# Performance work log

Hardware: AMD Instinct MI355X
Metric: run time of the kernel (lower is better)

The kernel has to match this reference:

```python
import jax, jax.numpy as jnp
import numpy as np

EPS = 1e-20
TEMP = 0.07
PATCH = 64
STEP = 32  # patch_size * overlap(0.5)


def zero_softmax(x, eps=1e-5):
    # ZeroSoftmax: ((exp(x)-1)^2) / (sum + eps), maps x==0 -> exactly 0 weight
    e = jnp.square(jnp.exp(x) - 1.0)
    return e / (jnp.sum(e, axis=-1, keepdims=True) + eps)


def _scaling_mask(H, W, p, step):
    # constant overlap-count mask from CRW.compute_scaling_mask (static shapes)
    sm = np.zeros((H, W), np.float32)
    for i in range(0, H - step, step):
        for j in range(0, W - step, step):
            sm[i:i + p, j:j + p] += 1.0
    return jnp.asarray(sm)


def _window_sums(m, p, step):
    # m: (B,T,SP,H,W) -> sliding-window sums (B,T,SP,nH,nW) via integral image
    ii = jnp.cumsum(jnp.cumsum(m, axis=-2), axis=-1)
    ii = jnp.pad(ii, ((0, 0), (0, 0), (0, 0), (1, 0), (1, 0)))
    H = m.shape[-2]
    nH = (H - p) // step + 1
    lo = jnp.arange(nH) * step
    hi = lo + p
    r_hi = ii[..., hi, :]   # (B,T,SP,nH,W+1)
    r_lo = ii[..., lo, :]
    return r_hi[..., hi] - r_hi[..., lo] - r_lo[..., hi] + r_lo[..., lo]


def setup_inputs() -> dict:
    key = jax.random.key(0)
    k1, k2, k3 = jax.random.split(key, 3)
    B, T, H, W = 2, 4, 256, 256
    nH = (H - PATCH) // STEP + 1  # 7
    N = nH * nH                   # 49 patches
    Cenc, D, SP = 512, 128, 64
    feats = jax.random.normal(k1, (B, N, Cenc, T), jnp.float32)
    W_head = jax.random.normal(k2, (Cenc, D), jnp.float32) / np.sqrt(Cenc)
    sp_mask = jax.random.randint(k3, (B, T, H, W), 0, SP, jnp.int32)
    return {"feats": feats, "W_head": W_head, "sp_mask": sp_mask, "max_sp_num": SP}


def reference(feats, W_head, sp_mask, max_sp_num):
    B, N, Cenc, T = feats.shape
    H, W = sp_mask.shape[-2:]
    SP = max_sp_num

    # --- pixels_to_nodes tail: projection head + L2 normalize over channel dim ---
    q = jnp.einsum('bnct,cd->bndt', feats, W_head)            # (B,N,128,T)
    nrm = jnp.maximum(jnp.linalg.norm(q, axis=2, keepdims=True), 1e-12)
    q = q / nrm
    q = jnp.transpose(q, (0, 2, 3, 1))                        # (B,128,T,N)

    # --- patches_to_sp_embeddings: windowed superpixel pooling ---
    oh = (sp_mask[:, :, None, :, :] ==
          jnp.arange(SP, dtype=sp_mask.dtype)[None, None, :, None, None]
          ).astype(jnp.float32)                               # (B,T,SP,H,W)
    sm = _scaling_mask(H, W, PATCH, STEP)                     # (H,W)
    ws = _window_sums(oh / sm, PATCH, STEP)                   # (B,T,SP,nH,nW)
    denom = jnp.sum(oh, axis=(-1, -2)) + EPS                  # (B,T,SP)
    wts = jnp.transpose(ws, (0, 1, 3, 4, 2)) / denom[:, :, None, None, :]
    wts = wts.reshape(B, T, N, SP)                            # (B,T,N,SP)
    q_sp = jnp.einsum('bdtn,btns->bdts', q, wts)              # (B,128,T,SP)

    # --- affinity + zero_softmax stochastic matrices ---
    As = jnp.einsum('bdtn,bdtm->btnm', q_sp[:, :, :-1], q_sp[:, :, 1:])  # (B,T-1,SP,SP)
    A12 = zero_softmax(As / TEMP)
    A21 = zero_softmax(jnp.swapaxes(As, -1, -2) / TEMP)

    # --- palindrome random walks + cross-entropy to cycle-consistency targets ---
    tgt = jnp.tile(jnp.arange(SP), B)
    loss = jnp.float32(0.0)
    AAs = []
    for i in range(1, T - 1):
        mats = [A12[:, k] for k in range(i + 1)] + [A21[:, k] for k in range(i, -1, -1)]
        aa = mats[0]
        for m in mats[1:]:
            aa = aa @ m
        AAs.append(aa)
        logits = jnp.log(aa + EPS).reshape(B * SP, SP)
        logp = jax.nn.log_softmax(logits, axis=-1)
        loss = loss + jnp.mean(-logp[jnp.arange(B * SP), tgt])
    return loss, jnp.stack(AAs)
```

## Files before the change

### kernel.cpp

```cpp
#include <hip/hip_runtime.h>
#include <hip/hip_bf16.h>

constexpr int NWIN = 49;
constexpr int QLD  = 52;

constexpr int OFF_Q    = 26624;
constexpr int OFF_QSP  = 79872;
constexpr int OFF_A12T = 169984;
constexpr int OFF_A21  = 194560;
constexpr int OFF_A21T = 219136;
constexpr int OFF_R1T  = 251904;
constexpr int OFF_L    = 260096;
constexpr int OFF_BAR  = 276480;
constexpr int OFF_H    = 276608;

__global__ void __launch_bounds__(256, 1)
k_front(const int* __restrict__ mask, const float* __restrict__ feats,
        const float* __restrict__ Wh, float* __restrict__ h, float* __restrict__ q) {
    if (blockIdx.x < 98) {
        int bid = blockIdx.x;
        int n = bid % NWIN, b = bid / NWIN;
        __shared__ float4 f4[512];
        __shared__ float4 psum4[8 * 129];
        __shared__ float4 red4[2];
        const float4* fp4 = (const float4*)(feats + (size_t)(b * NWIN + n) * 2048);
        for (int i = threadIdx.x; i < 512; i += 256) f4[i] = fp4[i];
        __syncthreads();

        int dl = threadIdx.x & 31, ch = threadIdx.x >> 5;
        const float4* wh4 = (const float4*)Wh;
        float a0x=0.f,a0y=0.f,a0z=0.f,a0w=0.f;
        float a1x=0.f,a1y=0.f,a1z=0.f,a1w=0.f;
        float a2x=0.f,a2y=0.f,a2z=0.f,a2w=0.f;
        float a3x=0.f,a3y=0.f,a3z=0.f,a3w=0.f;
        int c0 = ch * 64;
        #pragma unroll 8
        for (int cc = 0; cc < 64; ++cc) {
            int c = c0 + cc;
            float4 w4 = wh4[c * 32 + dl];
            float4 fv = f4[c];
            a0x += fv.x * w4.x; a0y += fv.y * w4.x; a0z += fv.z * w4.x; a0w += fv.w * w4.x;
            a1x += fv.x * w4.y; a1y += fv.y * w4.y; a1z += fv.z * w4.y; a1w += fv.w * w4.y;
            a2x += fv.x * w4.z; a2y += fv.y * w4.z; a2z += fv.z * w4.z; a2w += fv.w * w4.z;
            a3x += fv.x * w4.w; a3y += fv.y * w4.w; a3z += fv.z * w4.w; a3w += fv.w * w4.w;
        }
        psum4[ch * 129 + dl * 4 + 0] = make_float4(a0x, a0y, a0z, a0w);
        psum4[ch * 129 + dl * 4 + 1] = make_float4(a1x, a1y, a1z, a1w);
        psum4[ch * 129 + dl * 4 + 2] = make_float4(a2x, a2y, a2z, a2w);
        psum4[ch * 129 + dl * 4 + 3] = make_float4(a3x, a3y, a3z, a3w);
        __syncthreads();

        float4 A;
        if (threadIdx.x < 128) {
            int d = threadIdx.x;
            A = psum4[d];
            #pragma unroll
            for (int c = 1; c < 8; ++c) {
                float4 p = psum4[c * 129 + d];
                A.x += p.x; A.y += p.y; A.z += p.z; A.w += p.w;
            }
            float sx = A.x * A.x, sy = A.y * A.y, sz = A.z * A.z, sw = A.w * A.w;
            for (int off = 32; off; off >>= 1) {
                sx += __shfl_down(sx, off); sy += __shfl_down(sy, off);
                sz += __shfl_down(sz, off); sw += __shfl_down(sw, off);
            }
            if ((threadIdx.x & 63) == 0) red4[threadIdx.x >> 6] = make_float4(sx, sy, sz, sw);
        }
        __syncthreads();
        if (threadIdx.x < 128) {
            float4 r0 = red4[0], r1 = red4[1];
            float ix = 1.f / fmaxf(sqrtf(r0.x + r1.x), 1e-12f);
            float iy = 1.f / fmaxf(sqrtf(r0.y + r1.y), 1e-12f);
            float iz = 1.f / fmaxf(sqrtf(r0.z + r1.z), 1e-12f);
            float iw = 1.f / fmaxf(sqrtf(r0.w + r1.w), 1e-12f);
            float* qb = q + (size_t)(b * 128 + (int)threadIdx.x) * 4 * QLD + n;
            qb[0 * QLD] = A.x * ix;
            qb[1 * QLD] = A.y * iy;
            qb[2 * QLD] = A.z * iz;
            qb[3 * QLD] = A.w * iw;
        }
    } else {
        int blkc = blockIdx.x - 98;
        int bt = blkc >> 6, cell = blkc & 63;
        int cy = cell >> 3, cx = cell & 7;
        __shared__ float loc[64];
        if (threadIdx.x < 64) loc[threadIdx.x] = 0.f;
        __syncthreads();
        const int* base = mask + bt * 65536 + (cy * 32) * 256 + cx * 32;
        #pragma unroll
        for (int it = 0; it < 4; ++it) {
            int idx = it * 256 + (int)threadIdx.x;
            int r = idx >> 5, c = idx & 31;
            int s = base[r * 256 + c];
            atomicAdd(&loc[s], 1.f);
        }
        __syncthreads();
        if (threadIdx.x < 64)
            h[(size_t)(bt * 64 + cell) * 64 + threadIdx.x] = loc[threadIdx.x];
    }
}

__global__ void k_qsp(const float* __restrict__ q, const float* __restrict__ hg,
                      float* __restrict__ qsp, float* __restrict__ out,
                      int* __restrict__ bar) {
    if (blockIdx.x == 0 && threadIdx.x < 4) {
        bar[threadIdx.x] = 0;
        if (threadIdx.x == 0) out[0] = 0.f;
    }
    int gid0 = blockIdx.x * 256;
    int t = (gid0 >> 13) & 3;
    int b = gid0 >> 15;
    int bt = b * 4 + t;
    int sbase = (gid0 >> 7) & 63;

    __shared__ float wrow[2][52];
    {
        int grp = threadIdx.x >> 7;
        int w = threadIdx.x & 127;
        if (w < 52) {
            float v = 0.f;
            if (w < 49) {
                int wy = w / 7, wx = w % 7;
                int s = sbase + grp;
                const float* hb = hg + (size_t)bt * 4096 + s;
                float wr0 = (wy >= 1 && wy <= 6) ? 0.5f : 1.f;
                float wr1 = (wy <= 5) ? 0.5f : 1.f;
                float wc0 = (wx >= 1 && wx <= 6) ? 0.5f : 1.f;
                float wc1 = (wx <= 5) ? 0.5f : 1.f;
                v = wr0 * wc0 * hb[(wy * 8 + wx) * 64]
                  + wr0 * wc1 * hb[(wy * 8 + wx + 1) * 64]
                  + wr1 * wc0 * hb[((wy + 1) * 8 + wx) * 64]
                  + wr1 * wc1 * hb[((wy + 1) * 8 + wx + 1) * 64];
            }
            wrow[grp][w] = v;
        }
    }
    __syncthreads();

    int tid = gid0 + threadIdx.x;
    int d = tid & 127;
    int s = (tid >> 7) & 63;
    const float4* qrow = (const float4*)(q + (size_t)((b * 128 + d) * 4 + t) * QLD);
    const float4* wr4 = (const float4*)wrow[threadIdx.x >> 7];
    float acc = 0.f, den = 0.f;
    #pragma unroll
    for (int i = 0; i < 13; ++i) {
        float4 w = wr4[i];
        float4 qv = qrow[i];
        den += w.x + w.y + w.z + w.w;
        acc += qv.x * w.x + qv.y * w.y + qv.z * w.z + qv.w * w.w;
    }
    int w = (s * 32 + ((d >> 2) ^ (s & 31))) * 4 + (d & 3);
    qsp[(size_t)bt * 8192 + w] = acc / (den + 1e-20f);
}


__device__ __forceinline__ void dump_mat(float* M, const float4* v) {
    #pragma unroll
    for (int it = 0; it < 4; ++it) {
        int idx = it * 256 + (int)threadIdx.x;
        int r = idx >> 4, c4 = (idx & 15) << 2;
        *(float4*)&M[r * 64 + (c4 ^ ((r & 15) << 2))] = v[it];
    }
}

__device__ __forceinline__ void stage1(float* M, const float* __restrict__ G) {
    const float4* g = (const float4*)G;
    float4 v[4];
    #pragma unroll
    for (int it = 0; it < 4; ++it) v[it] = g[it * 256 + (int)threadIdx.x];
    dump_mat(M, v);
}

__device__ __forceinline__ void mm256_sw(float* acc, const float* Ra, const float* Rb) {
    int tid = threadIdx.x;
    int nl = tid >> 4, ml = tid & 15;
    int sxa = nl << 2, sxb = ml << 2;
    #pragma unroll
    for (int i = 0; i < 16; ++i) acc[i] = 0.f;
    #pragma unroll 4
    for (int k0 = 0; k0 < 64; k0 += 4) {
        float4 av[4], bv[4];
        #pragma unroll
        for (int i = 0; i < 4; ++i)
            av[i] = *(const float4*)&Ra[(nl + 16 * i) * 64 + (k0 ^ sxa)];
        #pragma unroll
        for (int j = 0; j < 4; ++j)
            bv[j] = *(const float4*)&Rb[(ml + 16 * j) * 64 + (k0 ^ sxb)];
        #pragma unroll
        for (int i = 0; i < 4; ++i)
            #pragma unroll
            for (int j = 0; j < 4; ++j)
                acc[i * 4 + j] += av[i].x * bv[j].x + av[i].y * bv[j].y
                                + av[i].z * bv[j].z + av[i].w * bv[j].w;
    }
}

__device__ __forceinline__ void wr256_sw(float* M, const float* acc) {
    int nl = threadIdx.x >> 4, ml = threadIdx.x & 15;
    #pragma unroll
    for (int i = 0; i < 4; ++i)
        #pragma unroll
        for (int j = 0; j < 4; ++j) {
            int r = nl + 16 * i, k = ml + 16 * j;
            M[r * 64 + (((k & ~3) ^ ((r & 15) << 2)) | (k & 3))] = acc[i * 4 + j];
        }
}

__device__ __forceinline__ void store_mat(float* __restrict__ G, const float* acc) {
    int nl = threadIdx.x >> 4, ml = threadIdx.x & 15;
    #pragma unroll
    for (int i = 0; i < 4; ++i)
        #pragma unroll
        for (int j = 0; j < 4; ++j)
            G[(nl + 16 * i) * 64 + ml + 16 * j] = acc[i * 4 + j];
}

__device__ __forceinline__ void store_loss(const float* acc, float* __restrict__ aa,
                                           float* __restrict__ out, float* red) {
    int tid = threadIdx.x;
    int nl = tid >> 4, ml = tid & 15;
    #pragma unroll
    for (int i = 0; i < 4; ++i)
        #pragma unroll
        for (int j = 0; j < 4; ++j)
            aa[(nl + 16 * i) * 64 + (ml + 16 * j)] = acc[i * 4 + j];
    int l = tid & 63;
    float part = 0.f;
    #pragma unroll
    for (int i = 0; i < 4; ++i) {
        float rsum = acc[i * 4 + 0] + acc[i * 4 + 1] + acc[i * 4 + 2] + acc[i * 4 + 3];
        rsum += __shfl_down(rsum, 8, 16);
        rsum += __shfl_down(rsum, 4, 16);
        rsum += __shfl_down(rsum, 2, 16);
        rsum += __shfl_down(rsum, 1, 16);
        float dv = __shfl(acc[5 * i], (l & 48) | nl, 64);
        if ((l & 15) == 0) part += logf(rsum + 6.4e-19f) - logf(dv + 1e-20f);
    }
    for (int off = 32; off; off >>= 1) part += __shfl_down(part, off);
    if (l == 0) red[tid >> 6] = part;
    __syncthreads();
    if (tid == 0) atomicAdd(out, (red[0] + red[1] + red[2] + red[3]) * (1.f / 128.f));
}

__device__ __forceinline__ void gbar(int* cnt, int target) {
    __syncthreads();
    if (threadIdx.x == 0) {
        __threadfence();
        __hip_atomic_fetch_add(cnt, 1, __ATOMIC_ACQ_REL, __HIP_MEMORY_SCOPE_AGENT);
        while (__hip_atomic_load(cnt, __ATOMIC_ACQUIRE, __HIP_MEMORY_SCOPE_AGENT) < target)
            __builtin_amdgcn_s_sleep(2);
        __threadfence();
    }
    __syncthreads();
}

__global__ void __launch_bounds__(256, 1)
k_tail(const float* __restrict__ qsp,
       float* __restrict__ a12T, float* __restrict__ a21, float* __restrict__ a21T,
       float* __restrict__ wsR1T, float* __restrict__ wsL,
       float* __restrict__ out, int* __restrict__ bar) {
    __shared__ float SM[16384];
    float* M0 = SM;
    float* M1 = SM + 4096;
    float* M2 = SM + 8192;
    float* M3 = SM + 12288;
    const int tid = threadIdx.x;
    const int blk = blockIdx.x;
    const int t = blk % 3, b = blk / 3;

    {
        float4* qaT4 = (float4*)SM;
        float4* qbT4 = (float4*)SM + 2048;
        {
            const float4* gA = (const float4*)(qsp + (size_t)(b * 4 + t) * 8192);
            const float4* gB = (const float4*)(qsp + (size_t)(b * 4 + t + 1) * 8192);
            #pragma unroll
            for (int it = 0; it < 8; ++it) {
                int idx = it * 256 + tid;
                qaT4[idx] = gA[idx];
                qbT4[idx] = gB[idx];
            }
        }
        __syncthreads();

        const int nl = tid >> 4, ml = tid & 15;
        float acc[16];
        #pragma unroll
        for (int i = 0; i < 16; ++i) acc[i] = 0.f;
        #pragma unroll 8
        for (int k4 = 0; k4 < 32; ++k4) {
            float4 av[4], bv[4];
            #pragma unroll
            for (int i = 0; i < 4; ++i) { int n = nl + 16 * i; av[i] = qaT4[n * 32 + (k4 ^ (n & 31))]; }
            #pragma unroll
            for (int j = 0; j < 4; ++j) { int m = ml + 16 * j; bv[j] = qbT4[m * 32 + (k4 ^ (m & 31))]; }
            #pragma unroll
            for (int i = 0; i < 4; ++i)
                #pragma unroll
                for (int j = 0; j < 4; ++j)
                    acc[i * 4 + j] += av[i].x * bv[j].x + av[i].y * bv[j].y
                                    + av[i].z * bv[j].z + av[i].w * bv[j].w;
        }
        __syncthreads();

        float* eb = (float*)qaT4;
        float* rs = (float*)qbT4;
        float* cs = rs + 64;
        #pragma unroll
        for (int i = 0; i < 4; ++i)
            #pragma unroll
            for (int j = 0; j < 4; ++j) {
                int n = nl + 16 * i, m = ml + 16 * j;
                float x = acc[i * 4 + j] * (1.f / 0.07f);
                float e = expf(x) - 1.f;
                eb[n * 65 + m] = e * e;
            }
        __syncthreads();
        if (tid < 128) {
            int r = tid & 63; bool isrow = tid < 64;
            float a = 0.f;
            #pragma unroll
            for (int k = 0; k < 64; ++k) a += isrow ? eb[r * 65 + k] : eb[k * 65 + r];
            (isrow ? rs : cs)[r] = a + 1e-5f;
        }
        __syncthreads();
        float* p12T = a12T + (b * 3 + t) * 4096;
        float* p21  = a21  + (b * 3 + t) * 4096;
        float* p21T = a21T + (b * 3 + t) * 4096;
        #pragma unroll
        for (int i = 0; i < 4; ++i)
            #pragma unroll
            for (int j = 0; j < 4; ++j) {
                int n = nl + 16 * i, m = ml + 16 * j;
                float v   = eb[n * 65 + m];
                float v12 = v / rs[n];
                float v21 = v / cs[m];
                if (t == 0) {
                    M3[n * 64 + (((m & ~3) ^ ((n & 15) << 2)) | (m & 3))] = v12;
                    p21T[n * 64 + m] = v21;
                } else if (t == 1) {
                    p12T[m * 64 + n] = v12;
                    M3[m * 64 + (((n & ~3) ^ ((m & 15) << 2)) | (n & 3))] = v21;
                } else {
                    p12T[m * 64 + n] = v12;
                    p21 [m * 64 + n] = v21;
                }
            }
    }
    gbar(bar + 0, 6);
    if (t == 2) return;
    const bool odd = (t == 1);

    if (!odd) {
        stage1(M0, a12T + (b * 3 + 1) * 4096);
        __syncthreads();
        float accP[16];
        mm256_sw(accP, M3, M0);
        wr256_sw(M1, accP);
        stage1(M2, a12T + (b * 3 + 2) * 4096);
        __syncthreads();
        float accL[16];
        mm256_sw(accL, M1, M2);
        store_mat(wsL + b * 4096, accL);
    } else {
        stage1(M0, a21T + (b * 3 + 0) * 4096);
        __syncthreads();
        float accR[16];
        mm256_sw(accR, M0, M3);
        store_mat(wsR1T + b * 4096, accR);
        wr256_sw(M1, accR);
        stage1(M2, a21 + (b * 3 + 2) * 4096);
        __syncthreads();
        float accRT[16];
        mm256_sw(accRT, M1, M2);
        wr256_sw(M0, accRT);
    }
    gbar(bar + 1, 4);

    if (!odd) {
        stage1(M2, wsR1T + b * 4096);
        __syncthreads();
        float acc[16];
        mm256_sw(acc, M1, M2);
        store_loss(acc, out + 1 + b * 4096, out, M0);
    } else {
        stage1(M2, wsL + b * 4096);
        __syncthreads();
        float acc[16];
        mm256_sw(acc, M2, M0);
        store_loss(acc, out + 1 + (2 + b) * 4096, out, M1);
    }
}

extern "C" void kernel_launch(void* const* d_in, const int* in_sizes, int n_in,
                              void* d_out, int out_size, void* d_ws, size_t ws_size,
                              hipStream_t stream) {
    const float* feats = (const float*)d_in[0];
    const float* Wh    = (const float*)d_in[1];
    const int*   mask  = (const int*)d_in[2];
    float* out = (float*)d_out;
    float* ws  = (float*)d_ws;

    float* q       = ws + OFF_Q;
    float* qsp     = ws + OFF_QSP;
    float* a12T    = ws + OFF_A12T;
    float* a21     = ws + OFF_A21;
    float* a21T    = ws + OFF_A21T;
    float* wsR1T   = ws + OFF_R1T;
    float* wsL     = ws + OFF_L;
    float* h       = ws + OFF_H;
    int*   bar     = (int*)(ws + OFF_BAR);

    k_front<<<98 + 512, 256, 0, stream>>>(mask, feats, Wh, h, q);
    k_qsp<<<256, 256, 0, stream>>>(q, h, qsp, out, bar);
    k_tail<<<6, 256, 0, stream>>>(qsp, a12T, a21, a21T,
                                  wsR1T, wsL, out, bar);
}
```

Baseline: 100.1 us.

## Use half-block 64x64 matmuls and overlap next-operand staging with compute in tail kernel

The 64x64 matrix products in the tail kernel now run on only the first 128 threads, each computing a 8x4 register tile. The other 128 threads load the next operand matrix from global memory into shared memory at the same time, which removes one __syncthreads and hides load latency. The affinity GEMM is also moved to 128 threads. The risk is that half the threads sit idle during compute and per-thread register pressure doubles, so throughput per matmul may fall.

```diff
diff --git a/kernel.cpp b/kernel.cpp
--- a/kernel.cpp
+++ b/kernel.cpp
@@ -155,7 +155,11 @@
 }
 
 
-__device__ __forceinline__ void dump_mat(float* M, const float4* v) {
+__device__ __forceinline__ void stage1(float* M, const float* __restrict__ G) {
+    const float4* g = (const float4*)G;
+    float4 v[4];
+    #pragma unroll
+    for (int it = 0; it < 4; ++it) v[it] = g[it * 256 + (int)threadIdx.x];
     #pragma unroll
     for (int it = 0; it < 4; ++it) {
         int idx = it * 256 + (int)threadIdx.x;
@@ -164,31 +168,34 @@
     }
 }
 
-__device__ __forceinline__ void stage1(float* M, const float* __restrict__ G) {
+__device__ __forceinline__ void stage1_h(float* M, const float* __restrict__ G) {
+    int lt = (int)threadIdx.x - 128;
     const float4* g = (const float4*)G;
-    float4 v[4];
-    #pragma unroll
-    for (int it = 0; it < 4; ++it) v[it] = g[it * 256 + (int)threadIdx.x];
-    dump_mat(M, v);
-}
-
-__device__ __forceinline__ void mm256_sw(float* acc, const float* Ra, const float* Rb) {
-    int tid = threadIdx.x;
-    int nl = tid >> 4, ml = tid & 15;
-    int sxa = nl << 2, sxb = ml << 2;
-    #pragma unroll
-    for (int i = 0; i < 16; ++i) acc[i] = 0.f;
-    #pragma unroll 4
+    #pragma unroll
+    for (int it = 0; it < 8; ++it) {
+        int idx = it * 128 + lt;
+        int r = idx >> 4, c4 = (idx & 15) << 2;
+        *(float4*)&M[r * 64 + (c4 ^ ((r & 15) << 2))] = g[idx];
+    }
+}
+
+__device__ __forceinline__ void mm128_sw(float* acc, const float* Ra, const float* Rb) {
+    int lt = threadIdx.x;
+    int nl = lt >> 4, ml = lt & 15;
+    int sxa0 = nl << 2, sxa1 = (nl + 8) << 2, sxb = ml << 2;
+    #pragma unroll
+    for (int i = 0; i < 32; ++i) acc[i] = 0.f;
+    #pragma unroll 2
     for (int k0 = 0; k0 < 64; k0 += 4) {
-        float4 av[4], bv[4];
-        #pragma unroll
-        for (int i = 0; i < 4; ++i)
-            av[i] = *(const float4*)&Ra[(nl + 16 * i) * 64 + (k0 ^ sxa)];
+        float4 av[8], bv[4];
+        #pragma unroll
+        for (int i = 0; i < 8; ++i)
+            av[i] = *(const float4*)&Ra[(nl + 8 * i) * 64 + (k0 ^ ((i & 1) ? sxa1 : sxa0))];
         #pragma unroll
         for (int j = 0; j < 4; ++j)
             bv[j] = *(const float4*)&Rb[(ml + 16 * j) * 64 + (k0 ^ sxb)];
         #pragma unroll
-        for (int i = 0; i < 4; ++i)
+        for (int i = 0; i < 8; ++i)
             #pragma unroll
             for (int j = 0; j < 4; ++j)
                 acc[i * 4 + j] += av[i].x * bv[j].x + av[i].y * bv[j].y
@@ -196,51 +203,53 @@
     }
 }
 
-__device__ __forceinline__ void wr256_sw(float* M, const float* acc) {
+__device__ __forceinline__ void wr128_sw(float* M, const float* acc) {
     int nl = threadIdx.x >> 4, ml = threadIdx.x & 15;
     #pragma unroll
-    for (int i = 0; i < 4; ++i)
+    for (int i = 0; i < 8; ++i)
         #pragma unroll
         for (int j = 0; j < 4; ++j) {
-            int r = nl + 16 * i, k = ml + 16 * j;
+            int r = nl + 8 * i, k = ml + 16 * j;
             M[r * 64 + (((k & ~3) ^ ((r & 15) << 2)) | (k & 3))] = acc[i * 4 + j];
         }
 }
 
-__device__ __forceinline__ void store_mat(float* __restrict__ G, const float* acc) {
+__device__ __forceinline__ void store_mat128(float* __restrict__ G, const float* acc) {
     int nl = threadIdx.x >> 4, ml = threadIdx.x & 15;
     #pragma unroll
-    for (int i = 0; i < 4; ++i)
+    for (int i = 0; i < 8; ++i)
         #pragma unroll
         for (int j = 0; j < 4; ++j)
-            G[(nl + 16 * i) * 64 + ml + 16 * j] = acc[i * 4 + j];
-}
-
-__device__ __forceinline__ void store_loss(const float* acc, float* __restrict__ aa,
-                                           float* __restrict__ out, float* red) {
+            G[(nl + 8 * i) * 64 + ml + 16 * j] = acc[i * 4 + j];
+}
+
+__device__ __forceinline__ void store_loss128(const float* acc, float* __restrict__ aa,
+                                              float* __restrict__ out, float* red) {
     int tid = threadIdx.x;
-    int nl = tid >> 4, ml = tid & 15;
-    #pragma unroll
-    for (int i = 0; i < 4; ++i)
-        #pragma unroll
-        for (int j = 0; j < 4; ++j)
-            aa[(nl + 16 * i) * 64 + (ml + 16 * j)] = acc[i * 4 + j];
-    int l = tid & 63;
-    float part = 0.f;
-    #pragma unroll
-    for (int i = 0; i < 4; ++i) {
-        float rsum = acc[i * 4 + 0] + acc[i * 4 + 1] + acc[i * 4 + 2] + acc[i * 4 + 3];
-        rsum += __shfl_down(rsum, 8, 16);
-        rsum += __shfl_down(rsum, 4, 16);
-        rsum += __shfl_down(rsum, 2, 16);
-        rsum += __shfl_down(rsum, 1, 16);
-        float dv = __shfl(acc[5 * i], (l & 48) | nl, 64);
-        if ((l & 15) == 0) part += logf(rsum + 6.4e-19f) - logf(dv + 1e-20f);
-    }
-    for (int off = 32; off; off >>= 1) part += __shfl_down(part, off);
-    if (l == 0) red[tid >> 6] = part;
+    if (tid < 128) {
+        int nl = tid >> 4, ml = tid & 15;
+        #pragma unroll
+        for (int i = 0; i < 8; ++i)
+            #pragma unroll
+            for (int j = 0; j < 4; ++j)
+                aa[(nl + 8 * i) * 64 + ml + 16 * j] = acc[i * 4 + j];
+        int l = tid & 63;
+        float part = 0.f;
+        #pragma unroll
+        for (int i = 0; i < 8; ++i) {
+            float rsum = acc[i * 4 + 0] + acc[i * 4 + 1] + acc[i * 4 + 2] + acc[i * 4 + 3];
+            rsum += __shfl_down(rsum, 8, 16);
+            rsum += __shfl_down(rsum, 4, 16);
+            rsum += __shfl_down(rsum, 2, 16);
+            rsum += __shfl_down(rsum, 1, 16);
+            float dv = __shfl(acc[i * 4 + (i >> 1)], (l & 48) | (nl + 8 * (i & 1)), 64);
+            if ((l & 15) == 0) part += logf(rsum + 6.4e-19f) - logf(dv + 1e-20f);
+        }
+        for (int off = 32; off; off >>= 1) part += __shfl_down(part, off);
+        if (l == 0) red[tid >> 6] = part;
+    }
     __syncthreads();
-    if (tid == 0) atomicAdd(out, (red[0] + red[1] + red[2] + red[3]) * (1.f / 128.f));
+    if (tid == 0) atomicAdd(out, (red[0] + red[1]) * (1.f / 128.f));
 }
 
 __device__ __forceinline__ void gbar(int* cnt, int target) {
@@ -285,37 +294,47 @@
         __syncthreads();
 
         const int nl = tid >> 4, ml = tid & 15;
-        float acc[16];
-        #pragma unroll
-        for (int i = 0; i < 16; ++i) acc[i] = 0.f;
-        #pragma unroll 8
-        for (int k4 = 0; k4 < 32; ++k4) {
-            float4 av[4], bv[4];
-            #pragma unroll
-            for (int i = 0; i < 4; ++i) { int n = nl + 16 * i; av[i] = qaT4[n * 32 + (k4 ^ (n & 31))]; }
-            #pragma unroll
-            for (int j = 0; j < 4; ++j) { int m = ml + 16 * j; bv[j] = qbT4[m * 32 + (k4 ^ (m & 31))]; }
-            #pragma unroll
-            for (int i = 0; i < 4; ++i)
+        float acc[32];
+        if (tid < 128) {
+            #pragma unroll
+            for (int i = 0; i < 32; ++i) acc[i] = 0.f;
+            #pragma unroll 2
+            for (int k4 = 0; k4 < 32; ++k4) {
+                float4 av[8], bv[4];
                 #pragma unroll
-                for (int j = 0; j < 4; ++j)
-                    acc[i * 4 + j] += av[i].x * bv[j].x + av[i].y * bv[j].y
-                                    + av[i].z * bv[j].z + av[i].w * bv[j].w;
+                for (int i = 0; i < 8; ++i) {
+                    int n = nl + 8 * i;
+                    av[i] = qaT4[n * 32 + (k4 ^ (nl + 8 * (i & 3)))];
+                }
+                #pragma unroll
+                for (int j = 0; j < 4; ++j) {
+                    int m = ml + 16 * j;
+                    bv[j] = qbT4[m * 32 + (k4 ^ (ml + 16 * (j & 1)))];
+                }
+                #pragma unroll
+                for (int i = 0; i < 8; ++i)
+                    #pragma unroll
+                    for (int j = 0; j < 4; ++j)
+                        acc[i * 4 + j] += av[i].x * bv[j].x + av[i].y * bv[j].y
+                                        + av[i].z * bv[j].z + av[i].w * bv[j].w;
+            }
         }
         __syncthreads();
 
         float* eb = (float*)qaT4;
         float* rs = (float*)qbT4;
         float* cs = rs + 64;
-        #pragma unroll
-        for (int i = 0; i < 4; ++i)
-            #pragma unroll
-            for (int j = 0; j < 4; ++j) {
-                int n = nl + 16 * i, m = ml + 16 * j;
-                float x = acc[i * 4 + j] * (1.f / 0.07f);
-                float e = expf(x) - 1.f;
-                eb[n * 65 + m] = e * e;
-            }
+        if (tid < 128) {
+            #pragma unroll
+            for (int i = 0; i < 8; ++i)
+                #pragma unroll
+                for (int j = 0; j < 4; ++j) {
+                    int n = nl + 8 * i, m = ml + 16 * j;
+                    float x = acc[i * 4 + j] * (1.f / 0.07f);
+                    float e = expf(x) - 1.f;
+                    eb[n * 65 + m] = e * e;
+                }
+        }
         __syncthreads();
         if (tid < 128) {
             int r = tid & 63; bool isrow = tid < 64;
@@ -325,28 +344,31 @@
             (isrow ? rs : cs)[r] = a + 1e-5f;
         }
         __syncthreads();
-        float* p12T = a12T + (b * 3 + t) * 4096;
-        float* p21  = a21  + (b * 3 + t) * 4096;
-        float* p21T = a21T + (b * 3 + t) * 4096;
-        #pragma unroll
-        for (int i = 0; i < 4; ++i)
-            #pragma unroll
-            for (int j = 0; j < 4; ++j) {
-                int n = nl + 16 * i, m = ml + 16 * j;
-                float v   = eb[n * 65 + m];
-                float v12 = v / rs[n];
-                float v21 = v / cs[m];
-                if (t == 0) {
-                    M3[n * 64 + (((m & ~3) ^ ((n & 15) << 2)) | (m & 3))] = v12;
-                    p21T[n * 64 + m] = v21;
-                } else if (t == 1) {
-                    p12T[m * 64 + n] = v12;
-                    M3[m * 64 + (((n & ~3) ^ ((m & 15) << 2)) | (n & 3))] = v21;
-                } else {
-                    p12T[m * 64 + n] = v12;
-                    p21 [m * 64 + n] = v21;
+        {
+            int nl4 = tid >> 4, ml4 = tid & 15;
+            float* p12T = a12T + (b * 3 + t) * 4096;
+            float* p21  = a21  + (b * 3 + t) * 4096;
+            float* p21T = a21T + (b * 3 + t) * 4096;
+            #pragma unroll
+            for (int i = 0; i < 4; ++i)
+                #pragma unroll
+                for (int j = 0; j < 4; ++j) {
+                    int n = nl4 + 16 * i, m = ml4 + 16 * j;
+                    float v   = eb[n * 65 + m];
+                    float v12 = v / rs[n];
+                    float v21 = v / cs[m];
+                    if (t == 0) {
+                        M3[n * 64 + (((m & ~3) ^ ((n & 15) << 2)) | (m & 3))] = v12;
+                        p21T[n * 64 + m] = v21;
+                    } else if (t == 1) {
+                        p12T[m * 64 + n] = v12;
+                        M3[m * 64 + (((n & ~3) ^ ((m & 15) << 2)) | (n & 3))] = v21;
+                    } else {
+                        p12T[m * 64 + n] = v12;
+                        p21 [m * 64 + n] = v21;
+                    }
                 }
-            }
+        }
     }
     gbar(bar + 0, 6);
     if (t == 2) return;
@@ -355,41 +377,47 @@
     if (!odd) {
         stage1(M0, a12T + (b * 3 + 1) * 4096);
         __syncthreads();
-        float accP[16];
-        mm256_sw(accP, M3, M0);
-        wr256_sw(M1, accP);
-        stage1(M2, a12T + (b * 3 + 2) * 4096);
-        __syncthreads();
-        float accL[16];
-        mm256_sw(accL, M1, M2);
-        store_mat(wsL + b * 4096, accL);
+        float accP[32];
+        if (tid < 128) mm128_sw(accP, M3, M0);
+        else stage1_h(M2, a12T + (b * 3 + 2) * 4096);
+        if (tid < 128) wr128_sw(M1, accP);
+        __syncthreads();
+        float accL[32];
+        if (tid < 128) {
+            mm128_sw(accL, M1, M2);
+            store_mat128(wsL + b * 4096, accL);
+        }
     } else {
         stage1(M0, a21T + (b * 3 + 0) * 4096);
         __syncthreads();
-        float accR[16];
-        mm256_sw(accR, M0, M3);
-        store_mat(wsR1T + b * 4096, accR);
-        wr256_sw(M1, accR);
-        stage1(M2, a21 + (b * 3 + 2) * 4096);
-        __syncthreads();
-        float accRT[16];
-        mm256_sw(accRT, M1, M2);
-        wr256_sw(M0, accRT);
+        float accR[32];
+        if (tid < 128) mm128_sw(accR, M0, M3);
+        else stage1_h(M2, a21 + (b * 3 + 2) * 4096);
+        if (tid < 128) {
+            store_mat128(wsR1T + b * 4096, accR);
+            wr128_sw(M1, accR);
+        }
+        __syncthreads();
+        float accRT[32];
+        if (tid < 128) {
+            mm128_sw(accRT, M1, M2);
+            wr128_sw(M0, accRT);
+        }
     }
     gbar(bar + 1, 4);
 
     if (!odd) {
         stage1(M2, wsR1T + b * 4096);
         __syncthreads();
-        float acc[16];
-        mm256_sw(acc, M1, M2);
-        store_loss(acc, out + 1 + b * 4096, out, M0);
+        float acc[32];
+        if (tid < 128) mm128_sw(acc, M1, M2);
+        store_loss128(acc, out + 1 + b * 4096, out, M0);
     } else {
         stage1(M2, wsL + b * 4096);
         __syncthreads();
-        float acc[16];
-        mm256_sw(acc, M2, M0);
-        store_loss(acc, out + 1 + (2 + b) * 4096, out, M1);
+        float acc[32];
+        if (tid < 128) mm128_sw(acc, M2, M0);
+        store_loss128(acc, out + 1 + (2 + b) * 4096, out, M1);
     }
 }
 
```

Measured after the change: 106.8 us. +6.6%, slower.
